# Kernel tuning notes

Measured on AMD Instinct MI355X. Metric: run time of the kernel, lower is better.

## Reference

```python
import jax, jax.numpy as jnp
import numpy as np

CAPACITY_FACTOR = 1.25


def setup_inputs() -> dict:
    key = jax.random.key(0)
    k1, k2, k3, k4, k5, k6 = jax.random.split(key, 6)
    N, d, E, h = 8192, 1024, 8, 2816
    x = jax.random.normal(k1, (N, d), dtype=jnp.float32)
    topK_indices = jax.random.randint(k2, (N,), 0, E, dtype=jnp.int64)
    topK_scores = jax.random.uniform(k3, (N,), dtype=jnp.float32)
    Wg = jax.random.normal(k4, (E, d, h), dtype=jnp.float32) * 0.02
    Wu = jax.random.normal(k5, (E, d, h), dtype=jnp.float32) * 0.02
    Wd = jax.random.normal(k6, (E, h, d), dtype=jnp.float32) * 0.02
    return {"x": x, "topK_indices": topK_indices, "topK_scores": topK_scores,
            "Wg": Wg, "Wu": Wu, "Wd": Wd}


def reference(x, topK_indices, topK_scores, Wg, Wu, Wd):
    # x: [N, d] tokens; topK_indices: [N] top-1 expert ids; per-expert SwiGLU FFN.
    N, d = x.shape
    E = Wg.shape[0]
    capacity = int(CAPACITY_FACTOR * N / E)  # = 1280

    idx = topK_indices.astype(jnp.int32)
    onehot = jax.nn.one_hot(idx, E, dtype=jnp.int32)            # [N, E]
    # position of each token within its expert's queue (first-come-first-served)
    pos = jnp.sum((jnp.cumsum(onehot, axis=0) - 1) * onehot, axis=1)  # [N]
    kept = pos < capacity                                        # dropped tokens pass through

    # flat dispatch slot: expert*capacity + pos for kept tokens, overflow bucket otherwise
    slots = jnp.where(kept, idx * capacity + pos, E * capacity)  # [N]
    buf = jnp.zeros((E * capacity + 1, d), dtype=x.dtype).at[slots].set(x)
    xe = buf[: E * capacity].reshape(E, capacity, d)             # [E, C, d]

    # per-expert SwiGLU FFN (grouped GEMMs)
    hgate = jnp.einsum('ecd,edh->ech', xe, Wg)
    hup = jnp.einsum('ecd,edh->ech', xe, Wu)
    hact = jax.nn.silu(hgate) * hup
    out = jnp.einsum('ech,ehd->ecd', hact, Wd).reshape(E * capacity, d)
    out = jnp.concatenate([out, jnp.zeros((1, d), out.dtype)], axis=0)

    y_tok = out[slots]                                           # gather back per token
    # multiply_gate_scores=True: scale expert output by routing score; dropped -> identity
    y = jnp.where(kept[:, None], y_tok * topK_scores[:, None], x)
    return y
```

## Files before the change

kernel.cpp:

```cpp
#include <hip/hip_runtime.h>
#include <cstdint>
#include <cstddef>

#define N_TOK 8192
#define DIM   1024
#define NEXP  8
#define HID   2816
#define CAP   1280

typedef __bf16 bf16x8 __attribute__((ext_vector_type(8)));
typedef float  floatx4 __attribute__((ext_vector_type(4)));
typedef unsigned short u16x8 __attribute__((ext_vector_type(8)));

__device__ __forceinline__ unsigned short f2bf(float f) {
  return __builtin_bit_cast(unsigned short, (__bf16)f);
}

__device__ __forceinline__ void async16(void* lds, const void* g) {
  __builtin_amdgcn_global_load_lds(
      (const __attribute__((address_space(1))) void*)g,
      (__attribute__((address_space(3))) void*)lds, 16, 0, 0);
}

__global__ void route_kernel(const int* __restrict__ idx, int idx_stride,
                             int* __restrict__ slot,
                             int* __restrict__ slot_token,
                             int* __restrict__ counts) {
  __shared__ int hist[256][NEXP];
  const int t = threadIdx.x;
  int loc[NEXP];
#pragma unroll
  for (int e = 0; e < NEXP; e++) loc[e] = 0;
  const int base = t * 32;
  for (int i = 0; i < 32; i++) {
    int e = idx[(base + i) * idx_stride];
    loc[e]++;
  }
#pragma unroll
  for (int e = 0; e < NEXP; e++) hist[t][e] = loc[e];
  __syncthreads();
  if (t < NEXP) {
    int run = 0;
    for (int i = 0; i < 256; i++) { int v = hist[i][t]; hist[i][t] = run; run += v; }
    counts[t] = run < CAP ? run : CAP;
  }
  __syncthreads();
  int b2[NEXP];
#pragma unroll
  for (int e = 0; e < NEXP; e++) b2[e] = hist[t][e];
  for (int i = 0; i < 32; i++) {
    const int n = base + i;
    const int e = idx[n * idx_stride];
    const int p = b2[e]++;
    if (p < CAP) {
      const int s = e * CAP + p;
      slot[n] = s;
      slot_token[s] = n;
    } else {
      slot[n] = -1;
    }
  }
}

__global__ void dispatch_kernel(const float* __restrict__ x,
                                const int* __restrict__ slot,
                                unsigned short* __restrict__ xe,
                                float* __restrict__ y) {
  const int n = blockIdx.x;
  const int t = threadIdx.x;
  const int s = slot[n];
  const float4 v = ((const float4*)(x + (size_t)n * DIM))[t];
  if (s >= 0) {
    ushort4 b;
    b.x = f2bf(v.x); b.y = f2bf(v.y); b.z = f2bf(v.z); b.w = f2bf(v.w);
    ((ushort4*)(xe + (size_t)s * DIM))[t] = b;
  } else {
    ((float4*)(y + (size_t)n * DIM))[t] = v;
  }
}

__global__ __launch_bounds__(256)
void transpose_cvt(const float* __restrict__ in,
                   unsigned short* __restrict__ out,
                   const int R, const int C) {
  __shared__ float tile[64][65];
  const int e = blockIdx.z;
  const float* ib = in + (size_t)e * R * C;
  unsigned short* ob = out + (size_t)e * R * C;
  const int t = threadIdx.x;
  const int c0 = blockIdx.x * 64, r0 = blockIdx.y * 64;
  const int lr = t >> 4;
  const int lc = (t & 15) * 4;
#pragma unroll
  for (int i = 0; i < 4; i++) {
    const float4 v = *(const float4*)(ib + (size_t)(r0 + lr + i * 16) * C + c0 + lc);
    tile[lr + i * 16][lc + 0] = v.x;
    tile[lr + i * 16][lc + 1] = v.y;
    tile[lr + i * 16][lc + 2] = v.z;
    tile[lr + i * 16][lc + 3] = v.w;
  }
  __syncthreads();
  const int oc = t >> 2;
  const int sub = t & 3;
#pragma unroll
  for (int half = 0; half < 2; half++) {
    const int rch = sub + half * 4;
    u16x8 o;
#pragma unroll
    for (int j = 0; j < 8; j++) o[j] = f2bf(tile[rch * 8 + j][oc]);
    *(u16x8*)(ob + (size_t)(c0 + oc) * R + r0 + rch * 8) = o;
  }
}

__global__ __launch_bounds__(256)
void gateup_gemm(const unsigned short* __restrict__ A,
                 const unsigned short* __restrict__ Bg,
                 const unsigned short* __restrict__ Bu,
                 const int* __restrict__ counts,
                 unsigned short* __restrict__ hact) {
  const int bid = blockIdx.x;
  const int xcd = bid & 7;
  const int slot = bid >> 3;
  const int m = slot % 10;
  const int cgl = slot / 10;
  const int cg = xcd + 8 * cgl;
  const int n = cg % 44;
  const int e = cg / 44;

  const int cnt = counts[e];
  const int m0 = m * 128;
  if (m0 >= cnt) return;
  const int n0 = n * 64;

  __shared__ char smem[16384];

  const int t = threadIdx.x;
  const int lane = t & 63;
  const int w = t >> 6;
  const int wr = w >> 1;
  const int wc = w & 1;

  const int sr = t >> 2;
  const int sc = (t & 3) ^ ((sr >> 1) & 3);
  const unsigned short* aP  = A  + (size_t)e * CAP * DIM + (size_t)(m0 + sr) * DIM + sc * 8;
  const unsigned short* aP1 = aP + (size_t)64 * DIM;
  const unsigned short* bgP = Bg + (size_t)e * HID * DIM + (size_t)(n0 + sr) * DIM + sc * 8;
  const unsigned short* buP = Bu + (size_t)e * HID * DIM + (size_t)(n0 + sr) * DIM + sc * 8;
  char* lA0 = smem + t * 16;
  char* lA1 = smem + 4096 + t * 16;
  char* lBg = smem + 8192 + t * 16;
  char* lBu = smem + 12288 + t * 16;

  floatx4 accg[4][2] = {};
  floatx4 accu[4][2] = {};

  const int mrow = wr * 64 + (lane & 15);
  const int ncol = wc * 32 + (lane & 15);
  const int q = lane >> 4;
  const int kqA = ((q ^ ((mrow >> 1) & 3)) * 16);
  const int kqB = ((q ^ ((ncol >> 1) & 3)) * 16);

  for (int kk = 0; kk < DIM; kk += 32) {
    async16(lA0, aP); async16(lA1, aP1);
    async16(lBg, bgP); async16(lBu, buP);
    aP += 32; aP1 += 32; bgP += 32; buP += 32;
    __syncthreads();
    bf16x8 af[4], gf[2], uf[2];
#pragma unroll
    for (int i = 0; i < 4; i++)
      af[i] = *(const bf16x8*)(smem + (mrow + i * 16) * 64 + kqA);
#pragma unroll
    for (int i = 0; i < 2; i++) {
      gf[i] = *(const bf16x8*)(smem + 8192 + (ncol + i * 16) * 64 + kqB);
      uf[i] = *(const bf16x8*)(smem + 12288 + (ncol + i * 16) * 64 + kqB);
    }
#pragma unroll
    for (int mi = 0; mi < 4; mi++)
#pragma unroll
      for (int ni = 0; ni < 2; ni++) {
        accg[mi][ni] = __builtin_amdgcn_mfma_f32_16x16x32_bf16(
            af[mi], gf[ni], accg[mi][ni], 0, 0, 0);
        accu[mi][ni] = __builtin_amdgcn_mfma_f32_16x16x32_bf16(
            af[mi], uf[ni], accu[mi][ni], 0, 0, 0);
      }
    __syncthreads();
  }

  const int quad = lane >> 4;
  const int cl = lane & 15;
  unsigned short* ob = hact + (size_t)e * CAP * HID;
#pragma unroll
  for (int mi = 0; mi < 4; mi++)
#pragma unroll
    for (int r = 0; r < 4; r++) {
      const int row = m0 + wr * 64 + mi * 16 + quad * 4 + r;
      const size_t rb = (size_t)row * HID;
#pragma unroll
      for (int ni = 0; ni < 2; ni++) {
        const int col = n0 + wc * 32 + ni * 16 + cl;
        const float g = accg[mi][ni][r];
        const float u = accu[mi][ni][r];
        ob[rb + col] = f2bf(g / (1.0f + __expf(-g)) * u);
      }
    }
}

__global__ __launch_bounds__(256)
void down_gemm(const unsigned short* __restrict__ A,
               const unsigned short* __restrict__ Bt,
               const int* __restrict__ counts,
               const int* __restrict__ slot_token,
               const float* __restrict__ scores,
               float* __restrict__ y) {
  const int bid = blockIdx.x;
  const int xcd = bid & 7;
  const int slot = bid >> 3;
  const int m = slot % 10;
  const int cgl = slot / 10;
  const int cg = xcd + 8 * cgl;
  const int n = cg % 8;
  const int e = cg / 8;

  const int cnt = counts[e];
  const int m0 = m * 128;
  if (m0 >= cnt) return;
  const int n0 = n * 128;

  __shared__ char smem[16384];

  const int t = threadIdx.x;
  const int lane = t & 63;
  const int w = t >> 6;
  const int wr = w >> 1;
  const int wc = w & 1;

  const int sr = t >> 2;
  const int sc = (t & 3) ^ ((sr >> 1) & 3);
  const unsigned short* aP  = A + (size_t)e * CAP * HID + (size_t)(m0 + sr) * HID + sc * 8;
  const unsigned short* aP1 = aP + (size_t)64 * HID;
  const unsigned short* bP  = Bt + (size_t)e * DIM * HID + (size_t)(n0 + sr) * HID + sc * 8;
  const unsigned short* bP1 = bP + (size_t)64 * HID;
  char* lA0 = smem + t * 16;
  char* lA1 = smem + 4096 + t * 16;
  char* lB0 = smem + 8192 + t * 16;
  char* lB1 = smem + 12288 + t * 16;

  floatx4 acc[4][4] = {};

  const int mrow = wr * 64 + (lane & 15);
  const int ncol = wc * 64 + (lane & 15);
  const int q = lane >> 4;
  const int kqA = ((q ^ ((mrow >> 1) & 3)) * 16);
  const int kqB = ((q ^ ((ncol >> 1) & 3)) * 16);

  for (int kk = 0; kk < HID; kk += 32) {
    async16(lA0, aP); async16(lA1, aP1);
    async16(lB0, bP); async16(lB1, bP1);
    aP += 32; aP1 += 32; bP += 32; bP1 += 32;
    __syncthreads();
    bf16x8 af[4], bfr[4];
#pragma unroll
    for (int i = 0; i < 4; i++)
      af[i] = *(const bf16x8*)(smem + (mrow + i * 16) * 64 + kqA);
#pragma unroll
    for (int i = 0; i < 4; i++)
      bfr[i] = *(const bf16x8*)(smem + 8192 + (ncol + i * 16) * 64 + kqB);
#pragma unroll
    for (int mi = 0; mi < 4; mi++)
#pragma unroll
      for (int ni = 0; ni < 4; ni++)
        acc[mi][ni] = __builtin_amdgcn_mfma_f32_16x16x32_bf16(
            af[mi], bfr[ni], acc[mi][ni], 0, 0, 0);
    __syncthreads();
  }

  const int quad = lane >> 4;
  const int cl = lane & 15;
#pragma unroll
  for (int mi = 0; mi < 4; mi++)
#pragma unroll
    for (int r = 0; r < 4; r++) {
      const int row = m0 + wr * 64 + mi * 16 + quad * 4 + r;
      if (row < cnt) {
        const int tok = slot_token[e * CAP + row];
        const float s = scores[tok];
        float* yr = y + (size_t)tok * DIM;
#pragma unroll
        for (int ni = 0; ni < 4; ni++) {
          const int col = n0 + wc * 64 + ni * 16 + cl;
          yr[col] = acc[mi][ni][r] * s;
        }
      }
    }
}

extern "C" void kernel_launch(void* const* d_in, const int* in_sizes, int n_in,
                              void* d_out, int out_size, void* d_ws, size_t ws_size,
                              hipStream_t stream) {
  const float* x      = (const float*)d_in[0];
  const int*   idx    = (const int*)d_in[1];
  const float* scores = (const float*)d_in[2];
  const float* Wg     = (const float*)d_in[3];
  const float* Wu     = (const float*)d_in[4];
  const float* Wd     = (const float*)d_in[5];
  float* y = (float*)d_out;

  const int idx_stride = (in_sizes[1] == 2 * N_TOK) ? 2 : 1;

  char* ws = (char*)d_ws;
  size_t off = 0;
  auto alloc = [&](size_t b) -> char* {
    char* p = ws + off;
    off += (b + 255) & ~(size_t)255;
    return p;
  };
  int* counts            = (int*)alloc(NEXP * 4);
  int* slot              = (int*)alloc((size_t)N_TOK * 4);
  int* slot_token        = (int*)alloc((size_t)NEXP * CAP * 4);
  unsigned short* xe     = (unsigned short*)alloc((size_t)NEXP * CAP * DIM * 2);
  unsigned short* hact   = (unsigned short*)alloc((size_t)NEXP * CAP * HID * 2);
  unsigned short* wg_t   = (unsigned short*)alloc((size_t)NEXP * DIM * HID * 2);
  unsigned short* wu_t   = (unsigned short*)alloc((size_t)NEXP * DIM * HID * 2);
  unsigned short* wd_t   = (unsigned short*)alloc((size_t)NEXP * DIM * HID * 2);
  (void)ws_size; (void)n_in; (void)out_size;

  route_kernel<<<1, 256, 0, stream>>>(idx, idx_stride, slot, slot_token, counts);
  dispatch_kernel<<<N_TOK, 256, 0, stream>>>(x, slot, xe, y);

  transpose_cvt<<<dim3(HID / 64, DIM / 64, NEXP), 256, 0, stream>>>(Wg, wg_t, DIM, HID);
  transpose_cvt<<<dim3(HID / 64, DIM / 64, NEXP), 256, 0, stream>>>(Wu, wu_t, DIM, HID);
  transpose_cvt<<<dim3(DIM / 64, HID / 64, NEXP), 256, 0, stream>>>(Wd, wd_t, HID, DIM);

  gateup_gemm<<<8 * 44 * 10, 256, 0, stream>>>(xe, wg_t, wu_t, counts, hact);
  down_gemm<<<8 * 8 * 10, 256, 0, stream>>>(hact, wd_t, counts, slot_token, scores, y);
}
```

Baseline: 558.4 us.

## Rewrite expert GEMMs with 256-row tiles and double-buffered async LDS pipeline

Both grouped GEMMs now use 512-thread blocks with 256x128 output tiles and a K step of 64. Tile loads go through global_load_lds into double-buffered dynamic LDS, split into per-phase stages so loads overlap the MFMA work, with explicit vmcnt waits, raw barriers and s_setprio around the MFMA bursts. The aim is more operand reuse per LDS byte and hiding global-memory latency that the old single-buffered, syncthreads-bound loop exposed. In exchange, each block uses 96-128 KB of LDS, which limits occupancy. The grids also become smaller, so the partially filled last m-tile wastes more work.

Measured after the change: 586.4 us. +5.0%, slower.

```diff
diff --git a/kernel.cpp b/kernel.cpp
--- a/kernel.cpp
+++ b/kernel.cpp
@@ -20,6 +20,12 @@
   __builtin_amdgcn_global_load_lds(
       (const __attribute__((address_space(1))) void*)g,
       (__attribute__((address_space(3))) void*)lds, 16, 0, 0);
+}
+
+__device__ __forceinline__ void fence_barrier() {
+  asm volatile("" ::: "memory");
+  __builtin_amdgcn_s_barrier();
+  asm volatile("" ::: "memory");
 }
 
 __global__ void route_kernel(const int* __restrict__ idx, int idx_stride,
@@ -112,186 +118,260 @@
   }
 }
 
-__global__ __launch_bounds__(256)
-void gateup_gemm(const unsigned short* __restrict__ A,
-                 const unsigned short* __restrict__ Bg,
-                 const unsigned short* __restrict__ Bu,
-                 const int* __restrict__ counts,
-                 unsigned short* __restrict__ hact) {
+template <int MH, int BSTRIDE, class S, class TL>
+__device__ __forceinline__ void mm_phase(char* sm, int b, int boff,
+                                         int rowA, int rowB, int c0,
+                                         floatx4 (&acc)[8][2], S&& stage, TL&& tail) {
+  bf16x8 af[4][2], bfr[2][2];
+  {
+    const char* Ab = sm + b * BSTRIDE + MH * 16384 + rowA;
+    const char* Bb = sm + b * BSTRIDE + boff + rowB;
+#pragma unroll
+    for (int mi = 0; mi < 4; mi++) {
+      af[mi][0] = *(const bf16x8*)(Ab + mi * 2048 + c0);
+      af[mi][1] = *(const bf16x8*)(Ab + mi * 2048 + (c0 ^ 64));
+    }
+#pragma unroll
+    for (int ni = 0; ni < 2; ni++) {
+      bfr[ni][0] = *(const bf16x8*)(Bb + ni * 2048 + c0);
+      bfr[ni][1] = *(const bf16x8*)(Bb + ni * 2048 + (c0 ^ 64));
+    }
+  }
+  stage();
+  asm volatile("" ::: "memory");
+  __builtin_amdgcn_s_barrier();
+  asm volatile("s_waitcnt lgkmcnt(0)" ::: "memory");
+  __builtin_amdgcn_sched_barrier(0);
+  __builtin_amdgcn_s_setprio(1);
+#pragma unroll
+  for (int mi = 0; mi < 4; mi++)
+#pragma unroll
+    for (int ni = 0; ni < 2; ni++) {
+      acc[MH * 4 + mi][ni] = __builtin_amdgcn_mfma_f32_16x16x32_bf16(
+          af[mi][0], bfr[ni][0], acc[MH * 4 + mi][ni], 0, 0, 0);
+      acc[MH * 4 + mi][ni] = __builtin_amdgcn_mfma_f32_16x16x32_bf16(
+          af[mi][1], bfr[ni][1], acc[MH * 4 + mi][ni], 0, 0, 0);
+    }
+  __builtin_amdgcn_s_setprio(0);
+  tail();
+  asm volatile("" ::: "memory");
+  __builtin_amdgcn_s_barrier();
+  asm volatile("" ::: "memory");
+}
+
+__global__ __launch_bounds__(512, 2)
+void gateup_gemm8(const unsigned short* __restrict__ A,
+                  const unsigned short* __restrict__ Bg,
+                  const unsigned short* __restrict__ Bu,
+                  const int* __restrict__ counts,
+                  unsigned short* __restrict__ hact) {
+  extern __shared__ __align__(16) char smem[];
   const int bid = blockIdx.x;
   const int xcd = bid & 7;
-  const int slot = bid >> 3;
-  const int m = slot % 10;
-  const int cgl = slot / 10;
+  const int slotb = bid >> 3;
+  const int m = slotb % 5;
+  const int cgl = slotb / 5;
   const int cg = xcd + 8 * cgl;
-  const int n = cg % 44;
-  const int e = cg / 44;
+  const int n = cg % 22;
+  const int e = cg / 22;
 
   const int cnt = counts[e];
-  const int m0 = m * 128;
+  const int m0 = m * 256;
   if (m0 >= cnt) return;
-  const int n0 = n * 64;
-
-  __shared__ char smem[16384];
+  const int n0 = n * 128;
 
   const int t = threadIdx.x;
   const int lane = t & 63;
   const int w = t >> 6;
-  const int wr = w >> 1;
-  const int wc = w & 1;
-
-  const int sr = t >> 2;
-  const int sc = (t & 3) ^ ((sr >> 1) & 3);
-  const unsigned short* aP  = A  + (size_t)e * CAP * DIM + (size_t)(m0 + sr) * DIM + sc * 8;
-  const unsigned short* aP1 = aP + (size_t)64 * DIM;
-  const unsigned short* bgP = Bg + (size_t)e * HID * DIM + (size_t)(n0 + sr) * DIM + sc * 8;
-  const unsigned short* buP = Bu + (size_t)e * HID * DIM + (size_t)(n0 + sr) * DIM + sc * 8;
-  char* lA0 = smem + t * 16;
-  char* lA1 = smem + 4096 + t * 16;
-  char* lBg = smem + 8192 + t * 16;
-  char* lBu = smem + 12288 + t * 16;
-
-  floatx4 accg[4][2] = {};
-  floatx4 accu[4][2] = {};
-
-  const int mrow = wr * 64 + (lane & 15);
-  const int ncol = wc * 32 + (lane & 15);
+  const int wr = w >> 2;
+  const int wc = w & 3;
+  const int li = lane & 15;
   const int q = lane >> 4;
-  const int kqA = ((q ^ ((mrow >> 1) & 3)) * 16);
-  const int kqB = ((q ^ ((ncol >> 1) & 3)) * 16);
-
-  for (int kk = 0; kk < DIM; kk += 32) {
-    async16(lA0, aP); async16(lA1, aP1);
-    async16(lBg, bgP); async16(lBu, buP);
-    aP += 32; aP1 += 32; bgP += 32; buP += 32;
-    __syncthreads();
-    bf16x8 af[4], gf[2], uf[2];
-#pragma unroll
-    for (int i = 0; i < 4; i++)
-      af[i] = *(const bf16x8*)(smem + (mrow + i * 16) * 64 + kqA);
-#pragma unroll
-    for (int i = 0; i < 2; i++) {
-      gf[i] = *(const bf16x8*)(smem + 8192 + (ncol + i * 16) * 64 + kqB);
-      uf[i] = *(const bf16x8*)(smem + 12288 + (ncol + i * 16) * 64 + kqB);
-    }
+
+  const int sr8 = t >> 3;
+  const int cLog = (t & 7) ^ (sr8 & 7);
+  const unsigned short* aB  = A  + ((size_t)e * CAP + m0 + sr8) * DIM + cLog * 8;
+  const unsigned short* bgB = Bg + ((size_t)e * HID + n0 + sr8) * DIM + cLog * 8;
+  const unsigned short* buB = Bu + ((size_t)e * HID + n0 + sr8) * DIM + cLog * 8;
+
+  auto stageU = [&](int bb, int uoff, const unsigned short* s0, const unsigned short* s1) {
+    async16(smem + bb * 65536 + uoff + t * 16, s0);
+    async16(smem + bb * 65536 + uoff + 8192 + t * 16, s1);
+  };
+
+  const int rowA = (wr * 64 + li) * 128;
+  const int rowB = (wc * 32 + li) * 128;
+  const int c0 = (q ^ (li & 7)) * 16;
+
+  floatx4 accg[8][2] = {};
+  floatx4 accu[8][2] = {};
+
+  constexpr int NT = DIM / 64;
+
+  stageU(0, 0,     aB,                     aB + (size_t)64 * DIM);
+  stageU(0, 32768, bgB,                    bgB + (size_t)64 * DIM);
+  stageU(0, 49152, buB,                    buB + (size_t)64 * DIM);
+  stageU(0, 16384, aB + (size_t)128 * DIM, aB + (size_t)192 * DIM);
+  stageU(1, 0,     aB + 64,                aB + (size_t)64 * DIM + 64);
+  stageU(1, 32768, bgB + 64,               bgB + (size_t)64 * DIM + 64);
+  asm volatile("s_waitcnt vmcnt(4)" ::: "memory");
+  fence_barrier();
+
+#pragma unroll 2
+  for (int T = 0; T < NT; T++) {
+    const int b = T & 1;
+    const int bn = b ^ 1;
+    mm_phase<0, 65536>(smem, b, 32768, rowA, rowB, c0, accg,
+        [&] {
+          if (T + 1 < NT)
+            stageU(bn, 49152, buB + (T + 1) * 64,
+                              buB + (size_t)64 * DIM + (T + 1) * 64);
+        }, [] {});
+    mm_phase<0, 65536>(smem, b, 49152, rowA, rowB, c0, accu,
+        [&] {
+          if (T + 1 < NT)
+            stageU(bn, 16384, aB + (size_t)128 * DIM + (T + 1) * 64,
+                              aB + (size_t)192 * DIM + (T + 1) * 64);
+        }, [] {});
+    mm_phase<1, 65536>(smem, b, 32768, rowA, rowB, c0, accg,
+        [&] {
+          if (T + 2 < NT)
+            stageU(b, 0, aB + (T + 2) * 64,
+                         aB + (size_t)64 * DIM + (T + 2) * 64);
+        }, [] {});
+    mm_phase<1, 65536>(smem, b, 49152, rowA, rowB, c0, accu,
+        [&] {
+          if (T + 2 < NT)
+            stageU(b, 32768, bgB + (T + 2) * 64,
+                             bgB + (size_t)64 * DIM + (T + 2) * 64);
+        },
+        [&] {
+          if (T + 2 < NT)
+            asm volatile("s_waitcnt vmcnt(4)" ::: "memory");
+          else if (T + 1 < NT)
+            asm volatile("s_waitcnt vmcnt(0)" ::: "memory");
+        });
+  }
+
+  unsigned short* ob = hact + (size_t)e * CAP * HID;
+#pragma unroll
+  for (int mh = 0; mh < 2; mh++)
 #pragma unroll
     for (int mi = 0; mi < 4; mi++)
 #pragma unroll
-      for (int ni = 0; ni < 2; ni++) {
-        accg[mi][ni] = __builtin_amdgcn_mfma_f32_16x16x32_bf16(
-            af[mi], gf[ni], accg[mi][ni], 0, 0, 0);
-        accu[mi][ni] = __builtin_amdgcn_mfma_f32_16x16x32_bf16(
-            af[mi], uf[ni], accu[mi][ni], 0, 0, 0);
+      for (int r = 0; r < 4; r++) {
+        const int row = m0 + mh * 128 + wr * 64 + mi * 16 + q * 4 + r;
+        const size_t rb = (size_t)row * HID;
+#pragma unroll
+        for (int ni = 0; ni < 2; ni++) {
+          const int col = n0 + wc * 32 + ni * 16 + li;
+          const float g = accg[mh * 4 + mi][ni][r];
+          const float u = accu[mh * 4 + mi][ni][r];
+          ob[rb + col] = f2bf(g / (1.0f + __expf(-g)) * u);
+        }
       }
-    __syncthreads();
-  }
-
-  const int quad = lane >> 4;
-  const int cl = lane & 15;
-  unsigned short* ob = hact + (size_t)e * CAP * HID;
-#pragma unroll
-  for (int mi = 0; mi < 4; mi++)
-#pragma unroll
-    for (int r = 0; r < 4; r++) {
-      const int row = m0 + wr * 64 + mi * 16 + quad * 4 + r;
-      const size_t rb = (size_t)row * HID;
-#pragma unroll
-      for (int ni = 0; ni < 2; ni++) {
-        const int col = n0 + wc * 32 + ni * 16 + cl;
-        const float g = accg[mi][ni][r];
-        const float u = accu[mi][ni][r];
-        ob[rb + col] = f2bf(g / (1.0f + __expf(-g)) * u);
-      }
-    }
-}
-
-__global__ __launch_bounds__(256)
-void down_gemm(const unsigned short* __restrict__ A,
-               const unsigned short* __restrict__ Bt,
-               const int* __restrict__ counts,
-               const int* __restrict__ slot_token,
-               const float* __restrict__ scores,
-               float* __restrict__ y) {
+}
+
+__global__ __launch_bounds__(512, 2)
+void down_gemm8(const unsigned short* __restrict__ A,
+                const unsigned short* __restrict__ Bt,
+                const int* __restrict__ counts,
+                const int* __restrict__ slot_token,
+                const float* __restrict__ scores,
+                float* __restrict__ y) {
+  extern __shared__ __align__(16) char smem[];
   const int bid = blockIdx.x;
   const int xcd = bid & 7;
-  const int slot = bid >> 3;
-  const int m = slot % 10;
-  const int cgl = slot / 10;
+  const int slotb = bid >> 3;
+  const int m = slotb % 5;
+  const int cgl = slotb / 5;
   const int cg = xcd + 8 * cgl;
   const int n = cg % 8;
   const int e = cg / 8;
 
   const int cnt = counts[e];
-  const int m0 = m * 128;
+  const int m0 = m * 256;
   if (m0 >= cnt) return;
   const int n0 = n * 128;
-
-  __shared__ char smem[16384];
 
   const int t = threadIdx.x;
   const int lane = t & 63;
   const int w = t >> 6;
-  const int wr = w >> 1;
-  const int wc = w & 1;
-
-  const int sr = t >> 2;
-  const int sc = (t & 3) ^ ((sr >> 1) & 3);
-  const unsigned short* aP  = A + (size_t)e * CAP * HID + (size_t)(m0 + sr) * HID + sc * 8;
-  const unsigned short* aP1 = aP + (size_t)64 * HID;
-  const unsigned short* bP  = Bt + (size_t)e * DIM * HID + (size_t)(n0 + sr) * HID + sc * 8;
-  const unsigned short* bP1 = bP + (size_t)64 * HID;
-  char* lA0 = smem + t * 16;
-  char* lA1 = smem + 4096 + t * 16;
-  char* lB0 = smem + 8192 + t * 16;
-  char* lB1 = smem + 12288 + t * 16;
-
-  floatx4 acc[4][4] = {};
-
-  const int mrow = wr * 64 + (lane & 15);
-  const int ncol = wc * 64 + (lane & 15);
+  const int wr = w >> 2;
+  const int wc = w & 3;
+  const int li = lane & 15;
   const int q = lane >> 4;
-  const int kqA = ((q ^ ((mrow >> 1) & 3)) * 16);
-  const int kqB = ((q ^ ((ncol >> 1) & 3)) * 16);
-
-  for (int kk = 0; kk < HID; kk += 32) {
-    async16(lA0, aP); async16(lA1, aP1);
-    async16(lB0, bP); async16(lB1, bP1);
-    aP += 32; aP1 += 32; bP += 32; bP1 += 32;
-    __syncthreads();
-    bf16x8 af[4], bfr[4];
-#pragma unroll
-    for (int i = 0; i < 4; i++)
-      af[i] = *(const bf16x8*)(smem + (mrow + i * 16) * 64 + kqA);
-#pragma unroll
-    for (int i = 0; i < 4; i++)
-      bfr[i] = *(const bf16x8*)(smem + 8192 + (ncol + i * 16) * 64 + kqB);
+
+  const int sr8 = t >> 3;
+  const int cLog = (t & 7) ^ (sr8 & 7);
+  const unsigned short* aB = A  + ((size_t)e * CAP + m0 + sr8) * HID + cLog * 8;
+  const unsigned short* bB = Bt + ((size_t)e * DIM + n0 + sr8) * HID + cLog * 8;
+
+  auto stageU = [&](int bb, int uoff, const unsigned short* s0, const unsigned short* s1) {
+    async16(smem + bb * 49152 + uoff + t * 16, s0);
+    async16(smem + bb * 49152 + uoff + 8192 + t * 16, s1);
+  };
+
+  const int rowA = (wr * 64 + li) * 128;
+  const int rowB = (wc * 32 + li) * 128;
+  const int c0 = (q ^ (li & 7)) * 16;
+
+  floatx4 acc[8][2] = {};
+
+  constexpr int NT = HID / 64;
+
+  stageU(0, 0,     aB,                     aB + (size_t)64 * HID);
+  stageU(0, 32768, bB,                     bB + (size_t)64 * HID);
+  stageU(0, 16384, aB + (size_t)128 * HID, aB + (size_t)192 * HID);
+  stageU(1, 0,     aB + 64,                aB + (size_t)64 * HID + 64);
+  asm volatile("s_waitcnt vmcnt(2)" ::: "memory");
+  fence_barrier();
+
+#pragma unroll 2
+  for (int T = 0; T < NT; T++) {
+    const int b = T & 1;
+    const int bn = b ^ 1;
+    mm_phase<0, 49152>(smem, b, 32768, rowA, rowB, c0, acc,
+        [&] {
+          if (T + 1 < NT) {
+            stageU(bn, 16384, aB + (size_t)128 * HID + (T + 1) * 64,
+                              aB + (size_t)192 * HID + (T + 1) * 64);
+            stageU(bn, 32768, bB + (T + 1) * 64,
+                              bB + (size_t)64 * HID + (T + 1) * 64);
+          }
+        }, [] {});
+    mm_phase<1, 49152>(smem, b, 32768, rowA, rowB, c0, acc,
+        [&] {
+          if (T + 2 < NT)
+            stageU(b, 0, aB + (T + 2) * 64,
+                         aB + (size_t)64 * HID + (T + 2) * 64);
+        },
+        [&] {
+          if (T + 2 < NT)
+            asm volatile("s_waitcnt vmcnt(2)" ::: "memory");
+          else if (T + 1 < NT)
+            asm volatile("s_waitcnt vmcnt(0)" ::: "memory");
+        });
+  }
+
+#pragma unroll
+  for (int mh = 0; mh < 2; mh++)
 #pragma unroll
     for (int mi = 0; mi < 4; mi++)
 #pragma unroll
-      for (int ni = 0; ni < 4; ni++)
-        acc[mi][ni] = __builtin_amdgcn_mfma_f32_16x16x32_bf16(
-            af[mi], bfr[ni], acc[mi][ni], 0, 0, 0);
-    __syncthreads();
-  }
-
-  const int quad = lane >> 4;
-  const int cl = lane & 15;
-#pragma unroll
-  for (int mi = 0; mi < 4; mi++)
-#pragma unroll
-    for (int r = 0; r < 4; r++) {
-      const int row = m0 + wr * 64 + mi * 16 + quad * 4 + r;
-      if (row < cnt) {
-        const int tok = slot_token[e * CAP + row];
-        const float s = scores[tok];
-        float* yr = y + (size_t)tok * DIM;
-#pragma unroll
-        for (int ni = 0; ni < 4; ni++) {
-          const int col = n0 + wc * 64 + ni * 16 + cl;
-          yr[col] = acc[mi][ni][r] * s;
+      for (int r = 0; r < 4; r++) {
+        const int row = m0 + mh * 128 + wr * 64 + mi * 16 + q * 4 + r;
+        if (row < cnt) {
+          const int tok = slot_token[e * CAP + row];
+          const float s = scores[tok];
+          float* yr = y + (size_t)tok * DIM;
+#pragma unroll
+          for (int ni = 0; ni < 2; ni++) {
+            const int col = n0 + wc * 32 + ni * 16 + li;
+            yr[col] = acc[mh * 4 + mi][ni][r] * s;
+          }
         }
       }
-    }
 }
 
 extern "C" void kernel_launch(void* const* d_in, const int* in_sizes, int n_in,
@@ -324,6 +404,15 @@
   unsigned short* wd_t   = (unsigned short*)alloc((size_t)NEXP * DIM * HID * 2);
   (void)ws_size; (void)n_in; (void)out_size;
 
+  static bool s_attr_done = false;
+  if (!s_attr_done) {
+    hipFuncSetAttribute((const void*)gateup_gemm8,
+                        hipFuncAttributeMaxDynamicSharedMemorySize, 131072);
+    hipFuncSetAttribute((const void*)down_gemm8,
+                        hipFuncAttributeMaxDynamicSharedMemorySize, 98304);
+    s_attr_done = true;
+  }
+
   route_kernel<<<1, 256, 0, stream>>>(idx, idx_stride, slot, slot_token, counts);
   dispatch_kernel<<<N_TOK, 256, 0, stream>>>(x, slot, xe, y);
 
@@ -331,6 +420,6 @@
   transpose_cvt<<<dim3(HID / 64, DIM / 64, NEXP), 256, 0, stream>>>(Wu, wu_t, DIM, HID);
   transpose_cvt<<<dim3(DIM / 64, HID / 64, NEXP), 256, 0, stream>>>(Wd, wd_t, HID, DIM);
 
-  gateup_gemm<<<8 * 44 * 10, 256, 0, stream>>>(xe, wg_t, wu_t, counts, hact);
-  down_gemm<<<8 * 8 * 10, 256, 0, stream>>>(hact, wd_t, counts, slot_token, scores, y);
-}
+  gateup_gemm8<<<8 * 22 * 5, 512, 131072, stream>>>(xe, wg_t, wu_t, counts, hact);
+  down_gemm8<<<8 * 8 * 5, 512, 98304, stream>>>(hact, wd_t, counts, slot_token, scores, y);
+}
```

## Add 4-stage async LDS pipelines to expert GEMMs and parallel-scan routing

Applied to the files above, without the earlier changes.

Both grouped GEMMs now use a four-buffer LDS ring filled by async global-to-LDS loads, prefetching three K-steps ahead. Fragment reads are double-buffered in registers and overlapped with the MFMAs using explicit waitcnt, barriers and setprio. The gate/up kernel moves to 512 threads with 256-row M tiles so each B tile is reused across more rows. Routing replaces the serial per-expert prefix loop with a parallel scan and indexes registers statically. The cost is much more shared memory and register pressure, and the correctness of the hand-written wait counts is fragile.

Measured after the change: 561.7 us. Within noise of the previous version (+0.6%).

```diff
diff --git a/kernel.cpp b/kernel.cpp
--- a/kernel.cpp
+++ b/kernel.cpp
@@ -20,6 +20,16 @@
   __builtin_amdgcn_global_load_lds(
       (const __attribute__((address_space(1))) void*)g,
       (__attribute__((address_space(3))) void*)lds, 16, 0, 0);
+}
+
+__device__ __forceinline__ void fence_barrier() {
+  asm volatile("" ::: "memory");
+  __builtin_amdgcn_s_barrier();
+  asm volatile("" ::: "memory");
+}
+
+__device__ __forceinline__ floatx4 mfma16(bf16x8 a, bf16x8 b, floatx4 c) {
+  return __builtin_amdgcn_mfma_f32_16x16x32_bf16(a, b, c, 0, 0, 0);
 }
 
 __global__ void route_kernel(const int* __restrict__ idx, int idx_stride,
@@ -33,25 +43,43 @@
   for (int e = 0; e < NEXP; e++) loc[e] = 0;
   const int base = t * 32;
   for (int i = 0; i < 32; i++) {
-    int e = idx[(base + i) * idx_stride];
-    loc[e]++;
-  }
-#pragma unroll
-  for (int e = 0; e < NEXP; e++) hist[t][e] = loc[e];
+    const int e = idx[(base + i) * idx_stride];
+#pragma unroll
+    for (int k = 0; k < NEXP; k++) loc[k] += (e == k) ? 1 : 0;
+  }
+  int v[NEXP];
+#pragma unroll
+  for (int e = 0; e < NEXP; e++) { v[e] = loc[e]; hist[t][e] = loc[e]; }
   __syncthreads();
+  for (int d = 1; d < 256; d <<= 1) {
+    int nb[NEXP];
+    const bool has = (t >= d);
+    if (has) {
+#pragma unroll
+      for (int e = 0; e < NEXP; e++) nb[e] = hist[t - d][e];
+    }
+    __syncthreads();
+    if (has) {
+#pragma unroll
+      for (int e = 0; e < NEXP; e++) { v[e] += nb[e]; hist[t][e] = v[e]; }
+    }
+    __syncthreads();
+  }
   if (t < NEXP) {
-    int run = 0;
-    for (int i = 0; i < 256; i++) { int v = hist[i][t]; hist[i][t] = run; run += v; }
-    counts[t] = run < CAP ? run : CAP;
-  }
-  __syncthreads();
+    const int tot = hist[255][t];
+    counts[t] = tot < CAP ? tot : CAP;
+  }
   int b2[NEXP];
 #pragma unroll
-  for (int e = 0; e < NEXP; e++) b2[e] = hist[t][e];
+  for (int e = 0; e < NEXP; e++) b2[e] = v[e] - loc[e];
   for (int i = 0; i < 32; i++) {
     const int n = base + i;
     const int e = idx[n * idx_stride];
-    const int p = b2[e]++;
+    int p = 0;
+#pragma unroll
+    for (int k = 0; k < NEXP; k++) {
+      if (e == k) { p = b2[k]; b2[k] = p + 1; }
+    }
     if (p < CAP) {
       const int s = e * CAP + p;
       slot[n] = s;
@@ -112,92 +140,132 @@
   }
 }
 
-__global__ __launch_bounds__(256)
-void gateup_gemm(const unsigned short* __restrict__ A,
-                 const unsigned short* __restrict__ Bg,
-                 const unsigned short* __restrict__ Bu,
-                 const int* __restrict__ counts,
-                 unsigned short* __restrict__ hact) {
+
+__global__ __launch_bounds__(512, 2)
+void gateup_gemm4(const unsigned short* __restrict__ A,
+                  const unsigned short* __restrict__ Bg,
+                  const unsigned short* __restrict__ Bu,
+                  const int* __restrict__ counts,
+                  unsigned short* __restrict__ hact) {
+  extern __shared__ __align__(16) char smem[];
   const int bid = blockIdx.x;
   const int xcd = bid & 7;
-  const int slot = bid >> 3;
-  const int m = slot % 10;
-  const int cgl = slot / 10;
+  const int slotb = bid >> 3;
+  const int m = slotb % 5;
+  const int cgl = slotb / 5;
   const int cg = xcd + 8 * cgl;
   const int n = cg % 44;
   const int e = cg / 44;
 
   const int cnt = counts[e];
-  const int m0 = m * 128;
+  const int m0 = m * 256;
   if (m0 >= cnt) return;
   const int n0 = n * 64;
-
-  __shared__ char smem[16384];
 
   const int t = threadIdx.x;
   const int lane = t & 63;
   const int w = t >> 6;
   const int wr = w >> 1;
   const int wc = w & 1;
-
-  const int sr = t >> 2;
-  const int sc = (t & 3) ^ ((sr >> 1) & 3);
-  const unsigned short* aP  = A  + (size_t)e * CAP * DIM + (size_t)(m0 + sr) * DIM + sc * 8;
-  const unsigned short* aP1 = aP + (size_t)64 * DIM;
-  const unsigned short* bgP = Bg + (size_t)e * HID * DIM + (size_t)(n0 + sr) * DIM + sc * 8;
-  const unsigned short* buP = Bu + (size_t)e * HID * DIM + (size_t)(n0 + sr) * DIM + sc * 8;
-  char* lA0 = smem + t * 16;
-  char* lA1 = smem + 4096 + t * 16;
-  char* lBg = smem + 8192 + t * 16;
-  char* lBu = smem + 12288 + t * 16;
+  const int li = lane & 15;
+  const int q = lane >> 4;
+
+  const int cphys = (((li & 1) * 4 + q) ^ (li >> 1)) * 16;
+  const int aoff0 = (wr * 32 + (li >> 1)) * 128 + cphys;
+  const int boff0 = 16384 + (wc * 16 + (li >> 1)) * 128 + cphys;
+
+  const int clog = (t & 7) ^ ((t >> 3) & 7);
+  const int kc = (clog & 3) * 8;
+  const int rloc = 2 * (t >> 3) + (clog >> 2);
+  const unsigned short* aSrc  = A + ((size_t)e * CAP + m0 + rloc) * DIM + kc;
+  const unsigned short* aSrc2 = aSrc + (size_t)128 * DIM;
+  const int rB = n0 + 2 * ((t >> 3) & 31) + (clog >> 2);
+  const unsigned short* bSrc =
+      ((t < 256) ? Bg : Bu) + ((size_t)e * HID + rB) * DIM + kc;
 
   floatx4 accg[4][2] = {};
   floatx4 accu[4][2] = {};
-
-  const int mrow = wr * 64 + (lane & 15);
-  const int ncol = wc * 32 + (lane & 15);
-  const int q = lane >> 4;
-  const int kqA = ((q ^ ((mrow >> 1) & 3)) * 16);
-  const int kqB = ((q ^ ((ncol >> 1) & 3)) * 16);
-
-  for (int kk = 0; kk < DIM; kk += 32) {
-    async16(lA0, aP); async16(lA1, aP1);
-    async16(lBg, bgP); async16(lBu, buP);
-    aP += 32; aP1 += 32; bgP += 32; buP += 32;
-    __syncthreads();
-    bf16x8 af[4], gf[2], uf[2];
-#pragma unroll
-    for (int i = 0; i < 4; i++)
-      af[i] = *(const bf16x8*)(smem + (mrow + i * 16) * 64 + kqA);
-#pragma unroll
-    for (int i = 0; i < 2; i++) {
-      gf[i] = *(const bf16x8*)(smem + 8192 + (ncol + i * 16) * 64 + kqB);
-      uf[i] = *(const bf16x8*)(smem + 12288 + (ncol + i * 16) * 64 + kqB);
-    }
-#pragma unroll
-    for (int mi = 0; mi < 4; mi++)
+  bf16x8 fA[8], fB[8];
+
+  constexpr int NTK = DIM / 32;
+
+#define GU_STAGE(TN)                                                        \
+  {                                                                         \
+    char* bb_ = smem + ((TN) & 3) * 24576;                                  \
+    const int ko_ = (TN) * 32;                                              \
+    async16(bb_ + t * 16, aSrc + ko_);                                      \
+    async16(bb_ + 8192 + t * 16, aSrc2 + ko_);                              \
+    async16(bb_ + 16384 + t * 16, bSrc + ko_);                              \
+  }
+
+#define GU_READF(DST, TN)                                                   \
+  {                                                                         \
+    const char* sb_ = smem + ((TN) & 3) * 24576;                            \
+    DST[0] = *(const bf16x8*)(sb_ + aoff0);                                 \
+    DST[1] = *(const bf16x8*)(sb_ + aoff0 + 1024);                          \
+    DST[2] = *(const bf16x8*)(sb_ + aoff0 + 2048);                          \
+    DST[3] = *(const bf16x8*)(sb_ + aoff0 + 3072);                          \
+    DST[4] = *(const bf16x8*)(sb_ + boff0);                                 \
+    DST[5] = *(const bf16x8*)(sb_ + boff0 + 1024);                          \
+    DST[6] = *(const bf16x8*)(sb_ + boff0 + 4096);                          \
+    DST[7] = *(const bf16x8*)(sb_ + boff0 + 5120);                          \
+  }
+
+#define GU_MFMA(CUR)                                                        \
+  {                                                                         \
+    __builtin_amdgcn_s_setprio(1);                                          \
+    _Pragma("unroll")                                                       \
+    for (int mi = 0; mi < 4; mi++) {                                        \
+      accg[mi][0] = mfma16(CUR[mi], CUR[4], accg[mi][0]);                   \
+      accg[mi][1] = mfma16(CUR[mi], CUR[5], accg[mi][1]);                   \
+      accu[mi][0] = mfma16(CUR[mi], CUR[6], accu[mi][0]);                   \
+      accu[mi][1] = mfma16(CUR[mi], CUR[7], accu[mi][1]);                   \
+    }                                                                       \
+    __builtin_amdgcn_s_setprio(0);                                          \
+  }
+
+#define GU_BODY(TN, CUR, NXT)                                               \
+  {                                                                         \
+    if ((TN) + 3 < NTK) GU_STAGE((TN) + 3);                                 \
+    if ((TN) + 1 < NTK) {                                                   \
+      if ((TN) + 3 < NTK)      asm volatile("s_waitcnt vmcnt(6)" ::: "memory"); \
+      else if ((TN) + 2 < NTK) asm volatile("s_waitcnt vmcnt(3)" ::: "memory"); \
+      else                     asm volatile("s_waitcnt vmcnt(0)" ::: "memory"); \
+      fence_barrier();                                                      \
+      GU_READF(NXT, (TN) + 1);                                              \
+      __builtin_amdgcn_sched_barrier(0);                                    \
+    }                                                                       \
+    GU_MFMA(CUR);                                                           \
+    asm volatile("s_waitcnt lgkmcnt(0)" ::: "memory");                      \
+    __builtin_amdgcn_sched_barrier(0);                                      \
+  }
+
+  GU_STAGE(0); GU_STAGE(1); GU_STAGE(2);
+  asm volatile("s_waitcnt vmcnt(6)" ::: "memory");
+  fence_barrier();
+  GU_READF(fA, 0);
+  asm volatile("s_waitcnt lgkmcnt(0)" ::: "memory");
+  __builtin_amdgcn_sched_barrier(0);
+
+  for (int T = 0; T < NTK; T += 2) {
+    GU_BODY(T, fA, fB);
+    GU_BODY(T + 1, fB, fA);
+  }
+#undef GU_BODY
+#undef GU_MFMA
+#undef GU_READF
+#undef GU_STAGE
+
+  unsigned short* ob = hact + (size_t)e * CAP * HID;
+#pragma unroll
+  for (int mi = 0; mi < 4; mi++)
+#pragma unroll
+    for (int r = 0; r < 4; r++) {
+      const int row = m0 + wr * 64 + mi * 16 + q * 4 + r;
+      const size_t rb = (size_t)row * HID;
 #pragma unroll
       for (int ni = 0; ni < 2; ni++) {
-        accg[mi][ni] = __builtin_amdgcn_mfma_f32_16x16x32_bf16(
-            af[mi], gf[ni], accg[mi][ni], 0, 0, 0);
-        accu[mi][ni] = __builtin_amdgcn_mfma_f32_16x16x32_bf16(
-            af[mi], uf[ni], accu[mi][ni], 0, 0, 0);
-      }
-    __syncthreads();
-  }
-
-  const int quad = lane >> 4;
-  const int cl = lane & 15;
-  unsigned short* ob = hact + (size_t)e * CAP * HID;
-#pragma unroll
-  for (int mi = 0; mi < 4; mi++)
-#pragma unroll
-    for (int r = 0; r < 4; r++) {
-      const int row = m0 + wr * 64 + mi * 16 + quad * 4 + r;
-      const size_t rb = (size_t)row * HID;
-#pragma unroll
-      for (int ni = 0; ni < 2; ni++) {
-        const int col = n0 + wc * 32 + ni * 16 + cl;
+        const int col = n0 + wc * 32 + ni * 16 + li;
         const float g = accg[mi][ni][r];
         const float u = accu[mi][ni][r];
         ob[rb + col] = f2bf(g / (1.0f + __expf(-g)) * u);
@@ -205,18 +273,19 @@
     }
 }
 
-__global__ __launch_bounds__(256)
-void down_gemm(const unsigned short* __restrict__ A,
-               const unsigned short* __restrict__ Bt,
-               const int* __restrict__ counts,
-               const int* __restrict__ slot_token,
-               const float* __restrict__ scores,
-               float* __restrict__ y) {
+__global__ __launch_bounds__(256, 2)
+void down_gemm4(const unsigned short* __restrict__ Ah,
+                const unsigned short* __restrict__ Bt,
+                const int* __restrict__ counts,
+                const int* __restrict__ slot_token,
+                const float* __restrict__ scores,
+                float* __restrict__ y) {
+  extern __shared__ __align__(16) char smem[];
   const int bid = blockIdx.x;
   const int xcd = bid & 7;
-  const int slot = bid >> 3;
-  const int m = slot % 10;
-  const int cgl = slot / 10;
+  const int slotb = bid >> 3;
+  const int m = slotb % 10;
+  const int cgl = slotb / 10;
   const int cg = xcd + 8 * cgl;
   const int n = cg % 8;
   const int e = cg / 8;
@@ -225,69 +294,111 @@
   const int m0 = m * 128;
   if (m0 >= cnt) return;
   const int n0 = n * 128;
-
-  __shared__ char smem[16384];
 
   const int t = threadIdx.x;
   const int lane = t & 63;
   const int w = t >> 6;
   const int wr = w >> 1;
   const int wc = w & 1;
-
-  const int sr = t >> 2;
-  const int sc = (t & 3) ^ ((sr >> 1) & 3);
-  const unsigned short* aP  = A + (size_t)e * CAP * HID + (size_t)(m0 + sr) * HID + sc * 8;
-  const unsigned short* aP1 = aP + (size_t)64 * HID;
-  const unsigned short* bP  = Bt + (size_t)e * DIM * HID + (size_t)(n0 + sr) * HID + sc * 8;
-  const unsigned short* bP1 = bP + (size_t)64 * HID;
-  char* lA0 = smem + t * 16;
-  char* lA1 = smem + 4096 + t * 16;
-  char* lB0 = smem + 8192 + t * 16;
-  char* lB1 = smem + 12288 + t * 16;
+  const int li = lane & 15;
+  const int q = lane >> 4;
+
+  const int cphys = (((li & 1) * 4 + q) ^ (li >> 1)) * 16;
+  const int aoff0 = (wr * 32 + (li >> 1)) * 128 + cphys;
+  const int boff0 = 8192 + (wc * 32 + (li >> 1)) * 128 + cphys;
+
+  const int clog = (t & 7) ^ ((t >> 3) & 7);
+  const int kc = (clog & 3) * 8;
+  const int rloc = 2 * (t >> 3) + (clog >> 2);
+  const unsigned short* aSrc  = Ah + ((size_t)e * CAP + m0 + rloc) * HID + kc;
+  const unsigned short* aSrc2 = aSrc + (size_t)64 * HID;
+  const unsigned short* bSrc  = Bt + ((size_t)e * DIM + n0 + rloc) * HID + kc;
+  const unsigned short* bSrc2 = bSrc + (size_t)64 * HID;
 
   floatx4 acc[4][4] = {};
-
-  const int mrow = wr * 64 + (lane & 15);
-  const int ncol = wc * 64 + (lane & 15);
-  const int q = lane >> 4;
-  const int kqA = ((q ^ ((mrow >> 1) & 3)) * 16);
-  const int kqB = ((q ^ ((ncol >> 1) & 3)) * 16);
-
-  for (int kk = 0; kk < HID; kk += 32) {
-    async16(lA0, aP); async16(lA1, aP1);
-    async16(lB0, bP); async16(lB1, bP1);
-    aP += 32; aP1 += 32; bP += 32; bP1 += 32;
-    __syncthreads();
-    bf16x8 af[4], bfr[4];
-#pragma unroll
-    for (int i = 0; i < 4; i++)
-      af[i] = *(const bf16x8*)(smem + (mrow + i * 16) * 64 + kqA);
-#pragma unroll
-    for (int i = 0; i < 4; i++)
-      bfr[i] = *(const bf16x8*)(smem + 8192 + (ncol + i * 16) * 64 + kqB);
-#pragma unroll
-    for (int mi = 0; mi < 4; mi++)
-#pragma unroll
-      for (int ni = 0; ni < 4; ni++)
-        acc[mi][ni] = __builtin_amdgcn_mfma_f32_16x16x32_bf16(
-            af[mi], bfr[ni], acc[mi][ni], 0, 0, 0);
-    __syncthreads();
-  }
-
-  const int quad = lane >> 4;
-  const int cl = lane & 15;
+  bf16x8 fA[8], fB[8];
+
+  constexpr int NTK = HID / 32;
+
+#define DN_STAGE(TN)                                                        \
+  {                                                                         \
+    char* bb_ = smem + ((TN) & 3) * 16384;                                  \
+    const int ko_ = (TN) * 32;                                              \
+    async16(bb_ + t * 16, aSrc + ko_);                                      \
+    async16(bb_ + 4096 + t * 16, aSrc2 + ko_);                              \
+    async16(bb_ + 8192 + t * 16, bSrc + ko_);                               \
+    async16(bb_ + 12288 + t * 16, bSrc2 + ko_);                             \
+  }
+
+#define DN_READF(DST, TN)                                                   \
+  {                                                                         \
+    const char* sb_ = smem + ((TN) & 3) * 16384;                            \
+    DST[0] = *(const bf16x8*)(sb_ + aoff0);                                 \
+    DST[1] = *(const bf16x8*)(sb_ + aoff0 + 1024);                          \
+    DST[2] = *(const bf16x8*)(sb_ + aoff0 + 2048);                          \
+    DST[3] = *(const bf16x8*)(sb_ + aoff0 + 3072);                          \
+    DST[4] = *(const bf16x8*)(sb_ + boff0);                                 \
+    DST[5] = *(const bf16x8*)(sb_ + boff0 + 1024);                          \
+    DST[6] = *(const bf16x8*)(sb_ + boff0 + 2048);                          \
+    DST[7] = *(const bf16x8*)(sb_ + boff0 + 3072);                          \
+  }
+
+#define DN_MFMA(CUR)                                                        \
+  {                                                                         \
+    __builtin_amdgcn_s_setprio(1);                                          \
+    _Pragma("unroll")                                                       \
+    for (int mi = 0; mi < 4; mi++) {                                        \
+      _Pragma("unroll")                                                     \
+      for (int ni = 0; ni < 4; ni++)                                        \
+        acc[mi][ni] = mfma16(CUR[mi], CUR[4 + ni], acc[mi][ni]);            \
+    }                                                                       \
+    __builtin_amdgcn_s_setprio(0);                                          \
+  }
+
+#define DN_BODY(TN, CUR, NXT)                                               \
+  {                                                                         \
+    if ((TN) + 3 < NTK) DN_STAGE((TN) + 3);                                 \
+    if ((TN) + 1 < NTK) {                                                   \
+      if ((TN) + 3 < NTK)      asm volatile("s_waitcnt vmcnt(8)" ::: "memory"); \
+      else if ((TN) + 2 < NTK) asm volatile("s_waitcnt vmcnt(4)" ::: "memory"); \
+      else                     asm volatile("s_waitcnt vmcnt(0)" ::: "memory"); \
+      fence_barrier();                                                      \
+      DN_READF(NXT, (TN) + 1);                                              \
+      __builtin_amdgcn_sched_barrier(0);                                    \
+    }                                                                       \
+    DN_MFMA(CUR);                                                           \
+    asm volatile("s_waitcnt lgkmcnt(0)" ::: "memory");                      \
+    __builtin_amdgcn_sched_barrier(0);                                      \
+  }
+
+  DN_STAGE(0); DN_STAGE(1); DN_STAGE(2);
+  asm volatile("s_waitcnt vmcnt(8)" ::: "memory");
+  fence_barrier();
+  DN_READF(fA, 0);
+  asm volatile("s_waitcnt lgkmcnt(0)" ::: "memory");
+  __builtin_amdgcn_sched_barrier(0);
+
+  for (int T = 0; T < NTK; T += 2) {
+    DN_BODY(T, fA, fB);
+    DN_BODY(T + 1, fB, fA);
+  }
+#undef DN_BODY
+#undef DN_MFMA
+#undef DN_READF
+#undef DN_STAGE
+
 #pragma unroll
   for (int mi = 0; mi < 4; mi++)
 #pragma unroll
     for (int r = 0; r < 4; r++) {
-      const int row = m0 + wr * 64 + mi * 16 + quad * 4 + r;
+      const int row = m0 + wr * 64 + mi * 16 + q * 4 + r;
       if (row < cnt) {
         const int tok = slot_token[e * CAP + row];
         const float s = scores[tok];
         float* yr = y + (size_t)tok * DIM;
 #pragma unroll
         for (int ni = 0; ni < 4; ni++) {
-          const int col = n0 + wc * 64 + ni * 16 + cl;
+          const int col = n0 + wc * 64 + ni * 16 + li;
           yr[col] = acc[mi][ni][r] * s;
         }
       }
@@ -324,6 +435,15 @@
   unsigned short* wd_t   = (unsigned short*)alloc((size_t)NEXP * DIM * HID * 2);
   (void)ws_size; (void)n_in; (void)out_size;
 
+  static bool s_attr_done = false;
+  if (!s_attr_done) {
+    hipFuncSetAttribute((const void*)gateup_gemm4,
+                        hipFuncAttributeMaxDynamicSharedMemorySize, 98304);
+    hipFuncSetAttribute((const void*)down_gemm4,
+                        hipFuncAttributeMaxDynamicSharedMemorySize, 65536);
+    s_attr_done = true;
+  }
+
   route_kernel<<<1, 256, 0, stream>>>(idx, idx_stride, slot, slot_token, counts);
   dispatch_kernel<<<N_TOK, 256, 0, stream>>>(x, slot, xe, y);
 
@@ -331,6 +451,6 @@
   transpose_cvt<<<dim3(HID / 64, DIM / 64, NEXP), 256, 0, stream>>>(Wu, wu_t, DIM, HID);
   transpose_cvt<<<dim3(DIM / 64, HID / 64, NEXP), 256, 0, stream>>>(Wd, wd_t, HID, DIM);
 
-  gateup_gemm<<<8 * 44 * 10, 256, 0, stream>>>(xe, wg_t, wu_t, counts, hact);
-  down_gemm<<<8 * 8 * 10, 256, 0, stream>>>(hact, wd_t, counts, slot_token, scores, y);
-}
+  gateup_gemm4<<<8 * 44 * 5, 512, 98304, stream>>>(xe, wg_t, wu_t, counts, hact);
+  down_gemm4<<<8 * 8 * 10, 256, 65536, stream>>>(hact, wd_t, counts, slot_token, scores, y);
+}
```
